# Kernel optimization log

Hardware: AMD Instinct MI355X
Metric: run time of the kernel (lower is better)

The kernel has to match this reference:

```python
import jax, jax.numpy as jnp
import numpy as np

DIM = 768
GP_NUM = 49


def setup_inputs() -> dict:
    key = jax.random.key(0)
    ks = jax.random.split(key, 7)
    b, n, d = 8, 2048, DIM
    s = d ** -0.5
    x = jax.random.normal(ks[0], (b, n, d), dtype=jnp.float32)
    W_qkv = jax.random.normal(ks[1], (d, 3 * d), dtype=jnp.float32) * s
    b_qkv = jnp.zeros((3 * d,), dtype=jnp.float32)
    W_proj = jax.random.normal(ks[2], (d, d), dtype=jnp.float32) * s
    b_proj = jnp.zeros((d,), dtype=jnp.float32)
    W_gp = jax.random.normal(ks[3], (d, GP_NUM), dtype=jnp.float32) * s
    alpha = jax.random.normal(ks[4], (), dtype=jnp.float32)
    return {"x": x, "W_qkv": W_qkv, "b_qkv": b_qkv, "W_proj": W_proj,
            "b_proj": b_proj, "W_gp": W_gp, "alpha": alpha}


def reference(x, W_qkv, b_qkv, W_proj, b_proj, W_gp, alpha):
    d = x.shape[-1]
    scale = d ** -0.5
    qkv = x @ W_qkv + b_qkv            # [b, n, 3d]
    q, k, v = jnp.split(qkv, 3, axis=-1)
    # full n x n attention scores
    attn_scores = jnp.einsum('bnd,bmd->bnm', q, k) * scale
    # group affinity: softmax(gelu(v @ W_gp)) then outer product over groups
    gw = jax.nn.softmax(jax.nn.gelu(v @ W_gp, approximate=False), axis=-1)  # [b, n, g]
    group_weight = jnp.einsum('bng,bmg->bnm', gw, gw)  # [b, n, n]
    attn_scores = jax.nn.softmax(attn_scores * group_weight, axis=-1)
    a = jax.nn.sigmoid(alpha)
    attn_weights = (1.0 - a) * attn_scores + a * group_weight
    out = jnp.einsum('bnm,bmd->bnd', attn_weights, v)
    return out @ W_proj + b_proj
```

## Files before the change

kernel.cpp:

```cpp
#include <hip/hip_runtime.h>
#include <hip/hip_bf16.h>
#include <math.h>

#define CB 8
#define CN 2048
#define CD 768
#define CDQKV 2304
#define NG 49
#define SLD 2112

typedef unsigned short ushort_t;
typedef __attribute__((ext_vector_type(8))) short bf16x8;
typedef __attribute__((ext_vector_type(4))) float f32x4;

__device__ __forceinline__ float bf2f(ushort_t u) {
    unsigned int x = ((unsigned int)u) << 16;
    return __builtin_bit_cast(float, x);
}
__device__ __forceinline__ ushort_t f2bf(float f) {
    unsigned int u = __builtin_bit_cast(unsigned int, f);
    u += 0x7fff + ((u >> 16) & 1);
    return (ushort_t)(u >> 16);
}
__device__ __forceinline__ ushort_t f2h(float f) {
    _Float16 h = (_Float16)f;
    return __builtin_bit_cast(ushort_t, h);
}
__device__ __forceinline__ float h2f(ushort_t u) {
    return (float)__builtin_bit_cast(_Float16, u);
}
__device__ __forceinline__ float sigmoidf_(float x) { return 1.f / (1.f + __expf(-x)); }

__device__ __forceinline__ void gload_lds16(const ushort_t* g, ushort_t* l) {
    __builtin_amdgcn_global_load_lds((const __attribute__((address_space(1))) void*)g,
                                     (__attribute__((address_space(3))) void*)l, 16, 0, 0);
}

__global__ void ws_fail_marker(float* out) {
    if (threadIdx.x == 0 && blockIdx.x == 0) out[0] = 31337.0f;
}

__global__ __launch_bounds__(256) void cast_bf16(const float* __restrict__ X,
                                                 ushort_t* __restrict__ XB, int n)
{
    int i = (blockIdx.x * 256 + threadIdx.x) * 8;
    if (i >= n) return;
    float4 a = *(const float4*)(X + i);
    float4 b = *(const float4*)(X + i + 4);
    ushort_t t[8];
    t[0] = f2bf(a.x); t[1] = f2bf(a.y); t[2] = f2bf(a.z); t[3] = f2bf(a.w);
    t[4] = f2bf(b.x); t[5] = f2bf(b.y); t[6] = f2bf(b.z); t[7] = f2bf(b.w);
    *(uint4*)(XB + i) = *(uint4*)t;
}

__global__ __launch_bounds__(256) void wt_kernel(const float* __restrict__ W,
                                                 ushort_t* __restrict__ WT,
                                                 int rows, int cols)
{
    __shared__ ushort_t tile[64][72];
    const int bx = blockIdx.x, by = blockIdx.y;
    const int t = threadIdx.x;
    const int r = t >> 2, cp = (t & 3) * 16;
    const float* src = W + (size_t)(by * 64 + r) * cols + bx * 64 + cp;
    ushort_t tmp[16];
#pragma unroll
    for (int i = 0; i < 16; i += 4) {
        float4 v = *(const float4*)(src + i);
        tmp[i + 0] = f2bf(v.x); tmp[i + 1] = f2bf(v.y);
        tmp[i + 2] = f2bf(v.z); tmp[i + 3] = f2bf(v.w);
    }
    *(uint4*)&tile[r][cp] = *(uint4*)tmp;
    *(uint4*)&tile[r][cp + 8] = *(uint4*)(tmp + 8);
    __syncthreads();
#pragma unroll
    for (int i = 0; i < 16; i++) tmp[i] = tile[cp + i][r];
    ushort_t* dst = WT + (size_t)(bx * 64 + r) * rows + by * 64 + cp;
    *(uint4*)dst = *(uint4*)tmp;
    *(uint4*)(dst + 8) = *(uint4*)(tmp + 8);
}

__global__ __launch_bounds__(256) void wgpt_kernel(const float* __restrict__ Wg,
                                                   ushort_t* __restrict__ WGPT)
{
    int idx = blockIdx.x * 256 + threadIdx.x;
    if (idx >= 64 * CD) return;
    int gg = idx / CD, k = idx % CD;
    WGPT[idx] = (gg < NG) ? f2bf(Wg[(size_t)k * NG + gg]) : (ushort_t)0;
}

#define STAGE256(dstA_, dstB_, kt_) do {                                       \
    _Pragma("unroll")                                                          \
    for (int _p = 0; _p < 4; _p++) {                                           \
        int _idx = _p * 512 + tid;                                             \
        int _row = _idx >> 3;                                                  \
        int _lsl = (_idx & 7) ^ (_row & 7);                                    \
        gload_lds16(Ab + (size_t)_row * LDA + (size_t)(kt_) * 64 + _lsl * 8,   \
                    (dstA_) + _idx * 8);                                       \
    }                                                                          \
    _Pragma("unroll")                                                          \
    for (int _p = 0; _p < 4; _p++) {                                           \
        int _idx = _p * 512 + tid;                                             \
        int _row = _idx >> 3;                                                  \
        int _lsl = (_idx & 7) ^ (_row & 7);                                    \
        gload_lds16(Bb + (size_t)_row * LDB + (size_t)(kt_) * 64 + _lsl * 8,   \
                    (dstB_) + _idx * 8);                                       \
    } } while (0)

template <int OUTMODE, int NK, int LDA, int LDB>
__global__ __launch_bounds__(512, 2) void gemm256(
    const ushort_t* __restrict__ Ag, const ushort_t* __restrict__ Bg,
    const float* __restrict__ bias,
    ushort_t* __restrict__ Qd, ushort_t* __restrict__ Kd, ushort_t* __restrict__ Vd,
    ushort_t* __restrict__ OB, float* __restrict__ OF)
{
    __shared__ __align__(16) ushort_t bufA[2][256 * 64];
    __shared__ __align__(16) ushort_t bufB[2][256 * 64];

    const int tid = threadIdx.x;
    const int lane = tid & 63;
    const int w = tid >> 6;
    const int c = lane & 15, g = lane >> 4;
    const int wr = w >> 2, wc = w & 3;

    const int per = gridDim.x >> 3;
    const int idx = (blockIdx.x & 7) * per + (blockIdx.x >> 3);
    const int mb = idx & 63;
    const int nb = idx >> 6;
    const int m0 = mb * 256;
    const int n0 = nb * 256;

    const ushort_t* Ab = Ag + (size_t)m0 * LDA;
    const ushort_t* Bb = (OUTMODE == 2)
        ? Bg + ((size_t)(m0 >> 11) * CD + n0) * LDB
        : Bg + (size_t)n0 * LDB;

    f32x4 acc[8][4];
#pragma unroll
    for (int i = 0; i < 8; i++)
#pragma unroll
        for (int j = 0; j < 4; j++) acc[i][j] = (f32x4){0.f, 0.f, 0.f, 0.f};

    STAGE256(bufA[0], bufB[0], 0);
    STAGE256(bufA[1], bufB[1], 1);

#pragma unroll 1
    for (int kt = 0; kt < NK; kt++) {
        const int cur = kt & 1;
        asm volatile("s_waitcnt vmcnt(8)" ::: "memory");
        __builtin_amdgcn_s_barrier();

        bf16x8 af[2][8], bf[2][4];
#pragma unroll
        for (int ks = 0; ks < 2; ks++) {
#pragma unroll
            for (int mf = 0; mf < 8; mf++) {
                int ra = wr * 128 + mf * 16 + c;
                int pa = (ks * 4 + g) ^ (ra & 7);
                af[ks][mf] = *(const bf16x8*)(&bufA[cur][0] + ra * 64 + pa * 8);
            }
#pragma unroll
            for (int nf = 0; nf < 4; nf++) {
                int rb = wc * 64 + nf * 16 + c;
                int pb = (ks * 4 + g) ^ (rb & 7);
                bf[ks][nf] = *(const bf16x8*)(&bufB[cur][0] + rb * 64 + pb * 8);
            }
        }
        asm volatile("s_waitcnt lgkmcnt(0)" ::: "memory");
        __builtin_amdgcn_s_barrier();
        if (kt + 2 < NK) STAGE256(bufA[cur], bufB[cur], kt + 2);

        __builtin_amdgcn_s_setprio(1);
#pragma unroll
        for (int ks = 0; ks < 2; ks++)
#pragma unroll
            for (int mf = 0; mf < 8; mf++)
#pragma unroll
                for (int nf = 0; nf < 4; nf++)
                    acc[mf][nf] = __builtin_amdgcn_mfma_f32_16x16x32_bf16(
                        af[ks][mf], bf[ks][nf], acc[mf][nf], 0, 0, 0);
        __builtin_amdgcn_s_setprio(0);
    }

    if (OUTMODE == 0) {
        const int seg = n0 / CD;
        const int nl0 = n0 % CD;
        ushort_t* dst = (seg == 0) ? Qd : (seg == 1) ? Kd : Vd;
#pragma unroll
        for (int nf = 0; nf < 4; nf++) {
            float bv = bias[n0 + wc * 64 + nf * 16 + c];
            int n = nl0 + wc * 64 + nf * 16 + c;
#pragma unroll
            for (int mf = 0; mf < 8; mf++)
#pragma unroll
                for (int r = 0; r < 4; r++) {
                    int m = m0 + wr * 128 + mf * 16 + g * 4 + r;
                    dst[(size_t)m * CD + n] = f2bf(acc[mf][nf][r] + bv);
                }
        }
    } else if (OUTMODE == 1) {
#pragma unroll
        for (int nf = 0; nf < 4; nf++) {
            int n = n0 + wc * 64 + nf * 16 + c;
            float bv = bias[n];
#pragma unroll
            for (int mf = 0; mf < 8; mf++)
#pragma unroll
                for (int r = 0; r < 4; r++) {
                    int m = m0 + wr * 128 + mf * 16 + g * 4 + r;
                    OF[(size_t)m * CD + n] = acc[mf][nf][r] + bv;
                }
        }
    } else {
#pragma unroll
        for (int nf = 0; nf < 4; nf++) {
            int n = n0 + wc * 64 + nf * 16 + c;
#pragma unroll
            for (int mf = 0; mf < 8; mf++)
#pragma unroll
                for (int r = 0; r < 4; r++) {
                    int m = m0 + wr * 128 + mf * 16 + g * 4 + r;
                    OB[(size_t)m * CD + n] = f2bf(acc[mf][nf][r]);
                }
        }
    }
}

#define GEN_STAGE(dstA_, dstB_, kt_, Abase_, Bbase_, lda_, ldb_) do {          \
    _Pragma("unroll")                                                          \
    for (int _p = 0; _p < 4; _p++) {                                           \
        int _idx = _p * 256 + tid;                                             \
        int _row = _idx >> 3;                                                  \
        int _lsl = (_idx & 7) ^ (_row & 7);                                    \
        gload_lds16((Abase_) + (size_t)_row * (lda_) + (size_t)(kt_) * 64 + _lsl * 8, \
                    (dstA_) + _idx * 8);                                       \
        gload_lds16((Bbase_) + (size_t)_row * (ldb_) + (size_t)(kt_) * 64 + _lsl * 8, \
                    (dstB_) + _idx * 8);                                       \
    } } while (0)

#define G_COMPUTE(srcA_, srcB_) do {                                           \
    _Pragma("unroll")                                                          \
    for (int _ks = 0; _ks < 2; _ks++) {                                        \
        bf16x8 _af[4], _bf[4];                                                 \
        _Pragma("unroll")                                                      \
        for (int _f = 0; _f < 4; _f++) {                                       \
            int _ra = wr * 64 + _f * 16 + c;                                   \
            int _pa = (_ks * 4 + g) ^ (_ra & 7);                               \
            _af[_f] = *(const bf16x8*)((srcA_) + _ra * 64 + _pa * 8);          \
            int _rb = wc * 64 + _f * 16 + c;                                   \
            int _pb = (_ks * 4 + g) ^ (_rb & 7);                               \
            _bf[_f] = *(const bf16x8*)((srcB_) + _rb * 64 + _pb * 8);          \
        }                                                                      \
        _Pragma("unroll")                                                      \
        for (int _mf = 0; _mf < 4; _mf++)                                      \
            _Pragma("unroll")                                                  \
            for (int _nf = 0; _nf < 4; _nf++)                                  \
                acc[_mf * 4 + _nf] = __builtin_amdgcn_mfma_f32_16x16x32_bf16(  \
                    _af[_mf], _bf[_nf], acc[_mf * 4 + _nf], 0, 0, 0);          \
    } } while (0)

#define STAGE_A128(dst_, base_, ld_, kt_) do {                                 \
    _Pragma("unroll")                                                          \
    for (int _p = 0; _p < 4; _p++) {                                           \
        int _idx = _p * 256 + tid;                                             \
        int _row = _idx >> 3;                                                  \
        int _lsl = (_idx & 7) ^ (_row & 7);                                    \
        gload_lds16((base_) + (size_t)_row * (ld_) + (size_t)(kt_) * 64 + _lsl * 8, \
                    (dst_) + _idx * 8);                                        \
    } } while (0)

#define STAGE_B64(dst_, base_, ld_, kt_) do {                                  \
    _Pragma("unroll")                                                          \
    for (int _p = 0; _p < 2; _p++) {                                           \
        int _idx = _p * 256 + tid;                                             \
        int _row = _idx >> 3;                                                  \
        int _lsl = (_idx & 7) ^ (_row & 7);                                    \
        gload_lds16((base_) + (size_t)_row * (ld_) + (size_t)(kt_) * 64 + _lsl * 8, \
                    (dst_) + _idx * 8);                                        \
    } } while (0)

#define N64_COMPUTE(srcA_, srcB_) do {                                         \
    _Pragma("unroll")                                                          \
    for (int _ks = 0; _ks < 2; _ks++) {                                        \
        bf16x8 _af[2], _bf[4];                                                 \
        _Pragma("unroll")                                                      \
        for (int _f = 0; _f < 2; _f++) {                                       \
            int _ra = w * 32 + _f * 16 + c;                                    \
            int _pa = (_ks * 4 + g) ^ (_ra & 7);                               \
            _af[_f] = *(const bf16x8*)((srcA_) + _ra * 64 + _pa * 8);          \
        }                                                                      \
        _Pragma("unroll")                                                      \
        for (int _f = 0; _f < 4; _f++) {                                       \
            int _rb = _f * 16 + c;                                             \
            int _pb = (_ks * 4 + g) ^ (_rb & 7);                               \
            _bf[_f] = *(const bf16x8*)((srcB_) + _rb * 64 + _pb * 8);          \
        }                                                                      \
        _Pragma("unroll")                                                      \
        for (int _mf = 0; _mf < 2; _mf++)                                      \
            _Pragma("unroll")                                                  \
            for (int _nf = 0; _nf < 4; _nf++)                                  \
                acc[_mf * 4 + _nf] = __builtin_amdgcn_mfma_f32_16x16x32_bf16(  \
                    _af[_mf], _bf[_nf], acc[_mf * 4 + _nf], 0, 0, 0);          \
    } } while (0)

__global__ __launch_bounds__(256, 2) void gw_gemm(
    const ushort_t* __restrict__ Vb, const ushort_t* __restrict__ WGPT,
    ushort_t* __restrict__ GWP, ushort_t* __restrict__ GWT)
{
    __shared__ __align__(16) ushort_t As[2][128 * 64];
    __shared__ __align__(16) ushort_t Bs[2][64 * 64];
    const int tid = threadIdx.x;
    const int lane = tid & 63;
    const int w = tid >> 6;
    const int c = lane & 15, g = lane >> 4;
    const int row0 = blockIdx.x * 128;
    const ushort_t* Ab = Vb + (size_t)row0 * CD;

    f32x4 acc[8];
#pragma unroll
    for (int i = 0; i < 8; i++) acc[i] = (f32x4){0.f, 0.f, 0.f, 0.f};

    STAGE_A128(As[0], Ab, CD, 0);
    STAGE_B64(Bs[0], WGPT, CD, 0);
    __syncthreads();
#pragma unroll 1
    for (int kt = 0; kt < 12; kt++) {
        const int cur = kt & 1;
        if (kt < 11) {
            STAGE_A128(As[cur ^ 1], Ab, CD, kt + 1);
            STAGE_B64(Bs[cur ^ 1], WGPT, CD, kt + 1);
        }
        N64_COMPUTE(As[cur], Bs[cur]);
        __syncthreads();
    }

    float gl[2][4][4];
#pragma unroll
    for (int mf = 0; mf < 2; mf++)
#pragma unroll
        for (int nf = 0; nf < 4; nf++) {
            int col = nf * 16 + c;
#pragma unroll
            for (int rr = 0; rr < 4; rr++) {
                float xx = acc[mf * 4 + nf][rr];
                float ge = 0.5f * xx * (1.f + erff(xx * 0.7071067811865475f));
                gl[mf][nf][rr] = (col < NG) ? ge : -1e30f;
            }
        }
#pragma unroll
    for (int mf = 0; mf < 2; mf++) {
#pragma unroll
        for (int rr = 0; rr < 4; rr++) {
            float m = fmaxf(fmaxf(gl[mf][0][rr], gl[mf][1][rr]),
                            fmaxf(gl[mf][2][rr], gl[mf][3][rr]));
#pragma unroll
            for (int s = 1; s < 16; s <<= 1) m = fmaxf(m, __shfl_xor(m, s, 64));
            float ssum = 0.f;
#pragma unroll
            for (int nf = 0; nf < 4; nf++) {
                int col = nf * 16 + c;
                float e = (col < NG) ? __expf(gl[mf][nf][rr] - m) : 0.f;
                gl[mf][nf][rr] = e;
                ssum += e;
            }
#pragma unroll
            for (int s = 1; s < 16; s <<= 1) ssum += __shfl_xor(ssum, s, 64);
            float inv = 1.f / ssum;
            int row = row0 + w * 32 + mf * 16 + g * 4 + rr;
            int bb = row >> 11, nn = row & 2047;
#pragma unroll
            for (int nf = 0; nf < 4; nf++) {
                int col = nf * 16 + c;
                ushort_t wv = f2bf(gl[mf][nf][rr] * inv);
                GWP[(size_t)row * 64 + col] = wv;
                GWT[((size_t)bb * 64 + col) * CN + nn] = wv;
            }
        }
    }
}

__global__ __launch_bounds__(256, 2) void z_gemm(
    ushort_t* __restrict__ VTt, const ushort_t* __restrict__ GWT)
{
    __shared__ __align__(16) ushort_t As[2][128 * 64];
    __shared__ __align__(16) ushort_t Bs[2][64 * 64];
    const int tid = threadIdx.x;
    const int lane = tid & 63;
    const int w = tid >> 6;
    const int c = lane & 15, g = lane >> 4;
    const int b = blockIdx.y;
    const int m0 = blockIdx.x * 128;
    const ushort_t* Ab = VTt + ((size_t)b * CD + m0) * SLD;
    const ushort_t* Bb = GWT + (size_t)b * 64 * CN;

    f32x4 acc[8];
#pragma unroll
    for (int i = 0; i < 8; i++) acc[i] = (f32x4){0.f, 0.f, 0.f, 0.f};

    STAGE_A128(As[0], Ab, SLD, 0);
    STAGE_B64(Bs[0], Bb, CN, 0);
    __syncthreads();
#pragma unroll 1
    for (int kt = 0; kt < 32; kt++) {
        const int cur = kt & 1;
        if (kt < 31) {
            STAGE_A128(As[cur ^ 1], Ab, SLD, kt + 1);
            STAGE_B64(Bs[cur ^ 1], Bb, CN, kt + 1);
        }
        N64_COMPUTE(As[cur], Bs[cur]);
        __syncthreads();
    }

#pragma unroll
    for (int mf = 0; mf < 2; mf++)
#pragma unroll
        for (int nf = 0; nf < 4; nf++) {
            int col = nf * 16 + c;
#pragma unroll
            for (int rr = 0; rr < 4; rr++) {
                int row = m0 + w * 32 + mf * 16 + g * 4 + rr;
                VTt[((size_t)b * CD + row) * SLD + 2048 + col] = f2bf(acc[mf * 4 + nf][rr]);
            }
        }
}

__global__ __launch_bounds__(256, 2) void s_gemm(
    const ushort_t* __restrict__ Qb, const ushort_t* __restrict__ Kb,
    const ushort_t* __restrict__ GWP, ushort_t* __restrict__ S)
{
    __shared__ __align__(16) ushort_t As[2][128 * 64];
    __shared__ __align__(16) ushort_t Bs[2][128 * 64];
    const int tid = threadIdx.x;
    const int lane = tid & 63;
    const int w = tid >> 6;
    const int c = lane & 15, g = lane >> 4;
    const int wr = w >> 1, wc = w & 1;
    const int b = blockIdx.z;
    const int m0 = blockIdx.x * 128;
    const int n0 = blockIdx.y * 128;
    const ushort_t* Ab = Qb + ((size_t)b * CN + m0) * CD;
    const ushort_t* Bb = Kb + ((size_t)b * CN + n0) * CD;

    f32x4 acc[16], gacc[16];
#pragma unroll
    for (int i = 0; i < 16; i++) {
        acc[i] = (f32x4){0.f, 0.f, 0.f, 0.f};
        gacc[i] = (f32x4){0.f, 0.f, 0.f, 0.f};
    }

    GEN_STAGE(As[0], Bs[0], 0, Ab, Bb, CD, CD);

    {
        const ushort_t* Gq = GWP + ((size_t)b * CN + m0) * 64;
        const ushort_t* Gk = GWP + ((size_t)b * CN + n0) * 64;
        bf16x8 gqf[2][4], gkf[2][4];
#pragma unroll
        for (int ks = 0; ks < 2; ks++)
#pragma unroll
            for (int f = 0; f < 4; f++) {
                gqf[ks][f] = *(const bf16x8*)(Gq + (size_t)(wr * 64 + f * 16 + c) * 64 + ks * 32 + g * 8);
                gkf[ks][f] = *(const bf16x8*)(Gk + (size_t)(wc * 64 + f * 16 + c) * 64 + ks * 32 + g * 8);
            }
#pragma unroll
        for (int ks = 0; ks < 2; ks++)
#pragma unroll
            for (int mf = 0; mf < 4; mf++)
#pragma unroll
                for (int nf = 0; nf < 4; nf++)
                    gacc[mf * 4 + nf] = __builtin_amdgcn_mfma_f32_16x16x32_bf16(
                        gqf[ks][mf], gkf[ks][nf], gacc[mf * 4 + nf], 0, 0, 0);
    }

    __syncthreads();
#pragma unroll 1
    for (int kt = 0; kt < 12; kt++) {
        const int cur = kt & 1;
        if (kt < 11) GEN_STAGE(As[cur ^ 1], Bs[cur ^ 1], kt + 1, Ab, Bb, CD, CD);
        G_COMPUTE(As[cur], Bs[cur]);
        __syncthreads();
    }

    ushort_t* Sb = S + ((size_t)b * CN + m0) * SLD + n0;
    const float scale = 0.03608439182435161f;
#pragma unroll
    for (int nf = 0; nf < 4; nf++) {
        int n = wc * 64 + nf * 16 + c;
#pragma unroll
        for (int mf = 0; mf < 4; mf++) {
#pragma unroll
            for (int r = 0; r < 4; r++) {
                int m = wr * 64 + mf * 16 + g * 4 + r;
                float z = acc[mf * 4 + nf][r] * scale * gacc[mf * 4 + nf][r];
                Sb[(size_t)m * SLD + n] = f2h(z);
            }
        }
    }
}

__global__ __launch_bounds__(256) void softmax_rows(ushort_t* __restrict__ SP,
                                                    const ushort_t* __restrict__ GWP,
                                                    const float* __restrict__ alpha_p)
{
    const int lane = threadIdx.x & 63;
    const int row = blockIdx.x * 4 + (threadIdx.x >> 6);
    ushort_t* rp = SP + (size_t)row * SLD;

    float v[32];
    float mx = -1e30f;
#pragma unroll
    for (int ch = 0; ch < 4; ch++) {
        uint4 u = *(const uint4*)(rp + ch * 512 + lane * 8);
        const unsigned int uu[4] = {u.x, u.y, u.z, u.w};
#pragma unroll
        for (int j = 0; j < 4; j++) {
            float a = h2f((ushort_t)(uu[j] & 0xffff));
            float bq = h2f((ushort_t)(uu[j] >> 16));
            v[ch * 8 + j * 2] = a;
            v[ch * 8 + j * 2 + 1] = bq;
            mx = fmaxf(mx, fmaxf(a, bq));
        }
    }
#pragma unroll
    for (int s = 32; s > 0; s >>= 1) mx = fmaxf(mx, __shfl_xor(mx, s, 64));
    float sum = 0.f;
#pragma unroll
    for (int i = 0; i < 32; i++) {
        v[i] = __expf(v[i] - mx);
        sum += v[i];
    }
#pragma unroll
    for (int s = 32; s > 0; s >>= 1) sum += __shfl_xor(sum, s, 64);
    const float aa = sigmoidf_(alpha_p[0]);
    float sc = (1.f - aa) / sum;
#pragma unroll
    for (int ch = 0; ch < 4; ch++) {
        ushort_t t[8];
#pragma unroll
        for (int j = 0; j < 8; j++) t[j] = f2bf(v[ch * 8 + j] * sc);
        *(uint4*)(rp + ch * 512 + lane * 8) = *(uint4*)t;
    }
    if (lane < 8) {
        const ushort_t* gp = GWP + (size_t)row * 64 + lane * 8;
        ushort_t t[8];
#pragma unroll
        for (int j = 0; j < 8; j++) t[j] = f2bf(aa * bf2f(gp[j]));
        *(uint4*)(rp + 2048 + lane * 8) = *(uint4*)t;
    }
}

__global__ __launch_bounds__(256) void vt_transpose(const ushort_t* __restrict__ VB,
                                                    ushort_t* __restrict__ VTt)
{
    __shared__ ushort_t tile[64][72];
    const int bx = blockIdx.x, by = blockIdx.y, b = blockIdx.z;
    const int t = threadIdx.x;
    const int r = t >> 2, cp = (t & 3) * 16;
    const ushort_t* src = VB + ((size_t)b * CN + bx * 64 + r) * CD + by * 64 + cp;
    *(uint4*)&tile[r][cp] = *(const uint4*)src;
    *(uint4*)&tile[r][cp + 8] = *(const uint4*)(src + 8);
    __syncthreads();
    ushort_t tmp[16];
#pragma unroll
    for (int i = 0; i < 16; i++) tmp[i] = tile[cp + i][r];
    ushort_t* dst = VTt + ((size_t)b * CD + by * 64 + r) * SLD + bx * 64 + cp;
    *(uint4*)dst = *(uint4*)tmp;
    *(uint4*)(dst + 8) = *(uint4*)(tmp + 8);
}

extern "C" void kernel_launch(void* const* d_in, const int* in_sizes, int n_in,
                              void* d_out, int out_size, void* d_ws, size_t ws_size,
                              hipStream_t stream) {
    const float* x      = (const float*)d_in[0];
    const float* W_qkv  = (const float*)d_in[1];
    const float* b_qkv  = (const float*)d_in[2];
    const float* W_proj = (const float*)d_in[3];
    const float* b_proj = (const float*)d_in[4];
    const float* W_gp   = (const float*)d_in[5];
    const float* alpha  = (const float*)d_in[6];
    float* out = (float*)d_out;

    const size_t BND    = (size_t)CB * CN * CD;
    const size_t SZ_BF  = BND * 2;
    const size_t SZ_VT  = (size_t)CB * CD * SLD * 2;
    const size_t SZ_WPT = (size_t)CD * CD * 2;
    const size_t SZ_GWP = (size_t)CB * CN * 64 * 2;
    const size_t SZ_GWT = (size_t)CB * 64 * CN * 2;
    const size_t SZ_WGPT= (size_t)64 * CD * 2;
    const size_t SZ_SP  = (size_t)CB * CN * SLD * 2;
    const size_t need = 4 * SZ_BF + SZ_VT + SZ_WPT + SZ_GWP + SZ_GWT + SZ_WGPT + SZ_SP;
    if (ws_size < need) {
        ws_fail_marker<<<1, 1, 0, stream>>>(out);
        return;
    }
    char* p = (char*)d_ws;
    ushort_t* qb   = (ushort_t*)p; p += SZ_BF;
    ushort_t* kb   = (ushort_t*)p; p += SZ_BF;
    ushort_t* vb   = (ushort_t*)p; p += SZ_BF;
    ushort_t* opb  = (ushort_t*)p; p += SZ_BF;
    ushort_t* vtb  = (ushort_t*)p; p += SZ_VT;
    ushort_t* wpt  = (ushort_t*)p; p += SZ_WPT;
    ushort_t* gwp  = (ushort_t*)p; p += SZ_GWP;
    ushort_t* gwt  = (ushort_t*)p; p += SZ_GWT;
    ushort_t* wgpt = (ushort_t*)p; p += SZ_WGPT;
    ushort_t* sp   = (ushort_t*)p; p += SZ_SP;
    ushort_t* xb  = sp;
    ushort_t* wqt = sp + BND;

    cast_bf16<<<dim3((int)(BND / 8 / 256)), 256, 0, stream>>>(x, xb, (int)BND);
    wt_kernel<<<dim3(36, 12), 256, 0, stream>>>(W_qkv, wqt, CD, CDQKV);
    wt_kernel<<<dim3(12, 12), 256, 0, stream>>>(W_proj, wpt, CD, CD);
    wgpt_kernel<<<dim3(192), 256, 0, stream>>>(W_gp, wgpt);
    gemm256<0, 12, CD, CD><<<dim3(576), 512, 0, stream>>>(
        xb, wqt, b_qkv, qb, kb, vb, nullptr, nullptr);
    gw_gemm<<<dim3(128), 256, 0, stream>>>(vb, wgpt, gwp, gwt);
    vt_transpose<<<dim3(32, 12, 8), 256, 0, stream>>>(vb, vtb);
    z_gemm<<<dim3(6, 8), 256, 0, stream>>>(vtb, gwt);
    s_gemm<<<dim3(16, 16, 8), 256, 0, stream>>>(qb, kb, gwp, sp);
    softmax_rows<<<dim3(4096), 256, 0, stream>>>(sp, gwp, alpha);
    gemm256<2, 33, SLD, SLD><<<dim3(192), 512, 0, stream>>>(
        sp, vtb, nullptr, nullptr, nullptr, nullptr, opb, nullptr);
    gemm256<1, 12, CD, CD><<<dim3(192), 512, 0, stream>>>(
        opb, wpt, b_proj, nullptr, nullptr, nullptr, nullptr, out);
}
```

Baseline: 361.0 us.

## Route QK^T score GEMM through 256-tile kernel and split main loop into phased MFMA quadrants

Removes the separate 128x128 s_gemm kernel and computes the QK^T scores with the 256x256, 512-thread gemm256 kernel in a new output mode. That mode computes the group-affinity product in the epilogue and writes the fused fp16 scores. The gemm256 inner loop is also restructured into four phases, interleaving LDS fragment reads of A and B sub-tiles with MFMA quadrants separated by barriers and priority hints. This is meant to overlap LDS reads with matrix math and to cut register pressure from holding all fragments at once. The cost is extra barriers per k-step, and the epilogue now computes the group-weight product per half-tile.

```diff
diff --git a/kernel.cpp b/kernel.cpp
--- a/kernel.cpp
+++ b/kernel.cpp
@@ -106,10 +106,49 @@
                     (dstB_) + _idx * 8);                                       \
     } } while (0)
 
+#define RD_A(SUB) do {                                                         \
+    _Pragma("unroll")                                                          \
+    for (int _ks = 0; _ks < 2; _ks++)                                          \
+        _Pragma("unroll")                                                      \
+        for (int _mf = 0; _mf < 4; _mf++) {                                    \
+            int _ra = wr * 128 + ((SUB) * 4 + _mf) * 16 + c;                   \
+            int _pa = (_ks * 4 + g) ^ (_ra & 7);                               \
+            aF[_ks][_mf] = *(const bf16x8*)(&bufA[cur][0] + _ra * 64 + _pa * 8); \
+        } } while (0)
+
+#define RD_B(SUB, DST) do {                                                    \
+    _Pragma("unroll")                                                          \
+    for (int _ks = 0; _ks < 2; _ks++)                                          \
+        _Pragma("unroll")                                                      \
+        for (int _nf = 0; _nf < 2; _nf++) {                                    \
+            int _rb = wc * 64 + ((SUB) * 2 + _nf) * 16 + c;                    \
+            int _pb = (_ks * 4 + g) ^ (_rb & 7);                               \
+            DST[_ks][_nf] = *(const bf16x8*)(&bufB[cur][0] + _rb * 64 + _pb * 8); \
+        } } while (0)
+
+#define QMF(ASUB, BSUB, BREG) do {                                             \
+    _Pragma("unroll")                                                          \
+    for (int _ks = 0; _ks < 2; _ks++)                                          \
+        _Pragma("unroll")                                                      \
+        for (int _mf = 0; _mf < 4; _mf++)                                      \
+            _Pragma("unroll")                                                  \
+            for (int _nf = 0; _nf < 2; _nf++)                                  \
+                acc[(ASUB) * 4 + _mf][(BSUB) * 2 + _nf] =                      \
+                    __builtin_amdgcn_mfma_f32_16x16x32_bf16(                   \
+                        aF[_ks][_mf], BREG[_ks][_nf],                          \
+                        acc[(ASUB) * 4 + _mf][(BSUB) * 2 + _nf], 0, 0, 0);     \
+    } while (0)
+
+#define PHASE_SYNC() do {                                                      \
+    __builtin_amdgcn_s_barrier();                                              \
+    asm volatile("s_waitcnt lgkmcnt(0)" ::: "memory");                         \
+    __builtin_amdgcn_sched_barrier(0);                                         \
+    } while (0)
+
 template <int OUTMODE, int NK, int LDA, int LDB>
 __global__ __launch_bounds__(512, 2) void gemm256(
     const ushort_t* __restrict__ Ag, const ushort_t* __restrict__ Bg,
-    const float* __restrict__ bias,
+    const float* __restrict__ bias, const ushort_t* __restrict__ Gw,
     ushort_t* __restrict__ Qd, ushort_t* __restrict__ Kd, ushort_t* __restrict__ Vd,
     ushort_t* __restrict__ OB, float* __restrict__ OF)
 {
@@ -124,15 +163,24 @@
 
     const int per = gridDim.x >> 3;
     const int idx = (blockIdx.x & 7) * per + (blockIdx.x >> 3);
-    const int mb = idx & 63;
-    const int nb = idx >> 6;
-    const int m0 = mb * 256;
-    const int n0 = nb * 256;
-
-    const ushort_t* Ab = Ag + (size_t)m0 * LDA;
-    const ushort_t* Bb = (OUTMODE == 2)
-        ? Bg + ((size_t)(m0 >> 11) * CD + n0) * LDB
-        : Bg + (size_t)n0 * LDB;
+
+    int bb = 0, m0, n0;
+    const ushort_t* Ab;
+    const ushort_t* Bb;
+    if (OUTMODE == 3) {
+        bb = idx >> 6;
+        m0 = ((idx >> 3) & 7) * 256;
+        n0 = (idx & 7) * 256;
+        Ab = Ag + ((size_t)bb * CN + m0) * LDA;
+        Bb = Bg + ((size_t)bb * CN + n0) * LDB;
+    } else {
+        m0 = (idx & 63) * 256;
+        n0 = (idx >> 6) * 256;
+        Ab = Ag + (size_t)m0 * LDA;
+        Bb = (OUTMODE == 2)
+            ? Bg + ((size_t)(m0 >> 11) * CD + n0) * LDB
+            : Bg + (size_t)n0 * LDB;
+    }
 
     f32x4 acc[8][4];
 #pragma unroll
@@ -142,6 +190,8 @@
 
     STAGE256(bufA[0], bufB[0], 0);
     STAGE256(bufA[1], bufB[1], 1);
+
+    bf16x8 aF[2][4], b0F[2][2], b1F[2][2];
 
 #pragma unroll 1
     for (int kt = 0; kt < NK; kt++) {
@@ -149,36 +199,20 @@
         asm volatile("s_waitcnt vmcnt(8)" ::: "memory");
         __builtin_amdgcn_s_barrier();
 
-        bf16x8 af[2][8], bf[2][4];
-#pragma unroll
-        for (int ks = 0; ks < 2; ks++) {
-#pragma unroll
-            for (int mf = 0; mf < 8; mf++) {
-                int ra = wr * 128 + mf * 16 + c;
-                int pa = (ks * 4 + g) ^ (ra & 7);
-                af[ks][mf] = *(const bf16x8*)(&bufA[cur][0] + ra * 64 + pa * 8);
-            }
-#pragma unroll
-            for (int nf = 0; nf < 4; nf++) {
-                int rb = wc * 64 + nf * 16 + c;
-                int pb = (ks * 4 + g) ^ (rb & 7);
-                bf[ks][nf] = *(const bf16x8*)(&bufB[cur][0] + rb * 64 + pb * 8);
-            }
-        }
-        asm volatile("s_waitcnt lgkmcnt(0)" ::: "memory");
+        RD_A(0); RD_B(0, b0F);
+        PHASE_SYNC();
+        __builtin_amdgcn_s_setprio(1); QMF(0, 0, b0F); __builtin_amdgcn_s_setprio(0);
+        __builtin_amdgcn_s_barrier();
+        RD_B(1, b1F);
+        PHASE_SYNC();
+        __builtin_amdgcn_s_setprio(1); QMF(0, 1, b1F); __builtin_amdgcn_s_setprio(0);
+        __builtin_amdgcn_s_barrier();
+        RD_A(1);
+        PHASE_SYNC();
+        __builtin_amdgcn_s_setprio(1); QMF(1, 1, b1F); __builtin_amdgcn_s_setprio(0);
         __builtin_amdgcn_s_barrier();
         if (kt + 2 < NK) STAGE256(bufA[cur], bufB[cur], kt + 2);
-
-        __builtin_amdgcn_s_setprio(1);
-#pragma unroll
-        for (int ks = 0; ks < 2; ks++)
-#pragma unroll
-            for (int mf = 0; mf < 8; mf++)
-#pragma unroll
-                for (int nf = 0; nf < 4; nf++)
-                    acc[mf][nf] = __builtin_amdgcn_mfma_f32_16x16x32_bf16(
-                        af[ks][mf], bf[ks][nf], acc[mf][nf], 0, 0, 0);
-        __builtin_amdgcn_s_setprio(0);
+        __builtin_amdgcn_s_setprio(1); QMF(1, 0, b0F); __builtin_amdgcn_s_setprio(0);
     }
 
     if (OUTMODE == 0) {
@@ -210,7 +244,7 @@
                     OF[(size_t)m * CD + n] = acc[mf][nf][r] + bv;
                 }
         }
-    } else {
+    } else if (OUTMODE == 2) {
 #pragma unroll
         for (int nf = 0; nf < 4; nf++) {
             int n = n0 + wc * 64 + nf * 16 + c;
@@ -222,41 +256,57 @@
                     OB[(size_t)m * CD + n] = f2bf(acc[mf][nf][r]);
                 }
         }
-    }
-}
-
-#define GEN_STAGE(dstA_, dstB_, kt_, Abase_, Bbase_, lda_, ldb_) do {          \
-    _Pragma("unroll")                                                          \
-    for (int _p = 0; _p < 4; _p++) {                                           \
-        int _idx = _p * 256 + tid;                                             \
-        int _row = _idx >> 3;                                                  \
-        int _lsl = (_idx & 7) ^ (_row & 7);                                    \
-        gload_lds16((Abase_) + (size_t)_row * (lda_) + (size_t)(kt_) * 64 + _lsl * 8, \
-                    (dstA_) + _idx * 8);                                       \
-        gload_lds16((Bbase_) + (size_t)_row * (ldb_) + (size_t)(kt_) * 64 + _lsl * 8, \
-                    (dstB_) + _idx * 8);                                       \
-    } } while (0)
-
-#define G_COMPUTE(srcA_, srcB_) do {                                           \
-    _Pragma("unroll")                                                          \
-    for (int _ks = 0; _ks < 2; _ks++) {                                        \
-        bf16x8 _af[4], _bf[4];                                                 \
-        _Pragma("unroll")                                                      \
-        for (int _f = 0; _f < 4; _f++) {                                       \
-            int _ra = wr * 64 + _f * 16 + c;                                   \
-            int _pa = (_ks * 4 + g) ^ (_ra & 7);                               \
-            _af[_f] = *(const bf16x8*)((srcA_) + _ra * 64 + _pa * 8);          \
-            int _rb = wc * 64 + _f * 16 + c;                                   \
-            int _pb = (_ks * 4 + g) ^ (_rb & 7);                               \
-            _bf[_f] = *(const bf16x8*)((srcB_) + _rb * 64 + _pb * 8);          \
-        }                                                                      \
-        _Pragma("unroll")                                                      \
-        for (int _mf = 0; _mf < 4; _mf++)                                      \
-            _Pragma("unroll")                                                  \
-            for (int _nf = 0; _nf < 4; _nf++)                                  \
-                acc[_mf * 4 + _nf] = __builtin_amdgcn_mfma_f32_16x16x32_bf16(  \
-                    _af[_mf], _bf[_nf], acc[_mf * 4 + _nf], 0, 0, 0);          \
-    } } while (0)
+    } else {
+        const float scale = 0.03608439182435161f;
+        const ushort_t* Gq = Gw + ((size_t)bb * CN + m0) * 64;
+        const ushort_t* Gk = Gw + ((size_t)bb * CN + n0) * 64;
+        ushort_t* Sb = OB + ((size_t)bb * CN + m0) * SLD + n0;
+#pragma unroll
+        for (int bh = 0; bh < 2; bh++) {
+            bf16x8 gkf[2][2];
+#pragma unroll
+            for (int ks = 0; ks < 2; ks++)
+#pragma unroll
+                for (int nf = 0; nf < 2; nf++)
+                    gkf[ks][nf] = *(const bf16x8*)(
+                        Gk + (size_t)(wc * 64 + (bh * 2 + nf) * 16 + c) * 64 + ks * 32 + g * 8);
+#pragma unroll
+            for (int ah = 0; ah < 2; ah++) {
+                bf16x8 gqf[2][4];
+#pragma unroll
+                for (int ks = 0; ks < 2; ks++)
+#pragma unroll
+                    for (int mf = 0; mf < 4; mf++)
+                        gqf[ks][mf] = *(const bf16x8*)(
+                            Gq + (size_t)(wr * 128 + (ah * 4 + mf) * 16 + c) * 64 + ks * 32 + g * 8);
+                f32x4 gq[4][2];
+#pragma unroll
+                for (int mf = 0; mf < 4; mf++)
+#pragma unroll
+                    for (int nf = 0; nf < 2; nf++) gq[mf][nf] = (f32x4){0.f, 0.f, 0.f, 0.f};
+#pragma unroll
+                for (int ks = 0; ks < 2; ks++)
+#pragma unroll
+                    for (int mf = 0; mf < 4; mf++)
+#pragma unroll
+                        for (int nf = 0; nf < 2; nf++)
+                            gq[mf][nf] = __builtin_amdgcn_mfma_f32_16x16x32_bf16(
+                                gqf[ks][mf], gkf[ks][nf], gq[mf][nf], 0, 0, 0);
+#pragma unroll
+                for (int mf = 0; mf < 4; mf++)
+#pragma unroll
+                    for (int nf = 0; nf < 2; nf++)
+#pragma unroll
+                        for (int r = 0; r < 4; r++) {
+                            int m = wr * 128 + (ah * 4 + mf) * 16 + g * 4 + r;
+                            int n = wc * 64 + (bh * 2 + nf) * 16 + c;
+                            float z = acc[ah * 4 + mf][bh * 2 + nf][r] * scale * gq[mf][nf][r];
+                            Sb[(size_t)m * SLD + n] = f2h(z);
+                        }
+            }
+        }
+    }
+}
 
 #define STAGE_A128(dst_, base_, ld_, kt_) do {                                 \
     _Pragma("unroll")                                                          \
@@ -423,79 +473,6 @@
         }
 }
 
-__global__ __launch_bounds__(256, 2) void s_gemm(
-    const ushort_t* __restrict__ Qb, const ushort_t* __restrict__ Kb,
-    const ushort_t* __restrict__ GWP, ushort_t* __restrict__ S)
-{
-    __shared__ __align__(16) ushort_t As[2][128 * 64];
-    __shared__ __align__(16) ushort_t Bs[2][128 * 64];
-    const int tid = threadIdx.x;
-    const int lane = tid & 63;
-    const int w = tid >> 6;
-    const int c = lane & 15, g = lane >> 4;
-    const int wr = w >> 1, wc = w & 1;
-    const int b = blockIdx.z;
-    const int m0 = blockIdx.x * 128;
-    const int n0 = blockIdx.y * 128;
-    const ushort_t* Ab = Qb + ((size_t)b * CN + m0) * CD;
-    const ushort_t* Bb = Kb + ((size_t)b * CN + n0) * CD;
-
-    f32x4 acc[16], gacc[16];
-#pragma unroll
-    for (int i = 0; i < 16; i++) {
-        acc[i] = (f32x4){0.f, 0.f, 0.f, 0.f};
-        gacc[i] = (f32x4){0.f, 0.f, 0.f, 0.f};
-    }
-
-    GEN_STAGE(As[0], Bs[0], 0, Ab, Bb, CD, CD);
-
-    {
-        const ushort_t* Gq = GWP + ((size_t)b * CN + m0) * 64;
-        const ushort_t* Gk = GWP + ((size_t)b * CN + n0) * 64;
-        bf16x8 gqf[2][4], gkf[2][4];
-#pragma unroll
-        for (int ks = 0; ks < 2; ks++)
-#pragma unroll
-            for (int f = 0; f < 4; f++) {
-                gqf[ks][f] = *(const bf16x8*)(Gq + (size_t)(wr * 64 + f * 16 + c) * 64 + ks * 32 + g * 8);
-                gkf[ks][f] = *(const bf16x8*)(Gk + (size_t)(wc * 64 + f * 16 + c) * 64 + ks * 32 + g * 8);
-            }
-#pragma unroll
-        for (int ks = 0; ks < 2; ks++)
-#pragma unroll
-            for (int mf = 0; mf < 4; mf++)
-#pragma unroll
-                for (int nf = 0; nf < 4; nf++)
-                    gacc[mf * 4 + nf] = __builtin_amdgcn_mfma_f32_16x16x32_bf16(
-                        gqf[ks][mf], gkf[ks][nf], gacc[mf * 4 + nf], 0, 0, 0);
-    }
-
-    __syncthreads();
-#pragma unroll 1
-    for (int kt = 0; kt < 12; kt++) {
-        const int cur = kt & 1;
-        if (kt < 11) GEN_STAGE(As[cur ^ 1], Bs[cur ^ 1], kt + 1, Ab, Bb, CD, CD);
-        G_COMPUTE(As[cur], Bs[cur]);
-        __syncthreads();
-    }
-
-    ushort_t* Sb = S + ((size_t)b * CN + m0) * SLD + n0;
-    const float scale = 0.03608439182435161f;
-#pragma unroll
-    for (int nf = 0; nf < 4; nf++) {
-        int n = wc * 64 + nf * 16 + c;
-#pragma unroll
-        for (int mf = 0; mf < 4; mf++) {
-#pragma unroll
-            for (int r = 0; r < 4; r++) {
-                int m = wr * 64 + mf * 16 + g * 4 + r;
-                float z = acc[mf * 4 + nf][r] * scale * gacc[mf * 4 + nf][r];
-                Sb[(size_t)m * SLD + n] = f2h(z);
-            }
-        }
-    }
-}
-
 __global__ __launch_bounds__(256) void softmax_rows(ushort_t* __restrict__ SP,
                                                     const ushort_t* __restrict__ GWP,
                                                     const float* __restrict__ alpha_p)
@@ -610,14 +587,15 @@
     wt_kernel<<<dim3(12, 12), 256, 0, stream>>>(W_proj, wpt, CD, CD);
     wgpt_kernel<<<dim3(192), 256, 0, stream>>>(W_gp, wgpt);
     gemm256<0, 12, CD, CD><<<dim3(576), 512, 0, stream>>>(
-        xb, wqt, b_qkv, qb, kb, vb, nullptr, nullptr);
+        xb, wqt, b_qkv, nullptr, qb, kb, vb, nullptr, nullptr);
     gw_gemm<<<dim3(128), 256, 0, stream>>>(vb, wgpt, gwp, gwt);
     vt_transpose<<<dim3(32, 12, 8), 256, 0, stream>>>(vb, vtb);
     z_gemm<<<dim3(6, 8), 256, 0, stream>>>(vtb, gwt);
-    s_gemm<<<dim3(16, 16, 8), 256, 0, stream>>>(qb, kb, gwp, sp);
+    gemm256<3, 12, CD, CD><<<dim3(512), 512, 0, stream>>>(
+        qb, kb, nullptr, gwp, nullptr, nullptr, nullptr, sp, nullptr);
     softmax_rows<<<dim3(4096), 256, 0, stream>>>(sp, gwp, alpha);
     gemm256<2, 33, SLD, SLD><<<dim3(192), 512, 0, stream>>>(
-        sp, vtb, nullptr, nullptr, nullptr, nullptr, opb, nullptr);
+        sp, vtb, nullptr, nullptr, nullptr, nullptr, nullptr, opb, nullptr);
     gemm256<1, 12, CD, CD><<<dim3(192), 512, 0, stream>>>(
-        opb, wpt, b_proj, nullptr, nullptr, nullptr, nullptr, out);
-}
+        opb, wpt, b_proj, nullptr, nullptr, nullptr, nullptr, nullptr, out);
+}
```

New measurement: 392.3 us. +8.7%, slower.
